# Performance work log

Measured on AMD Instinct MI355X. Metric: run time of the kernel, lower is better.

## Reference

```python
import jax, jax.numpy as jnp
import numpy as np

B, C, D, E = 2048, 64, 1024, 128
P_INT = 0.0  # p_int=0 -> intervention mask is all zeros (deterministic)


def setup_inputs() -> dict:
    key = jax.random.key(0)
    ks = jax.random.split(key, 16)
    s = lambda k, shape, fan: jax.random.normal(k, shape, jnp.float32) * (1.0 / np.sqrt(fan))
    return {
        "x": jax.random.normal(ks[0], (B, D), jnp.float32),
        "c_int": jax.random.uniform(ks[1], (B, C), jnp.float32),
        # stacked per-concept scorer MLP: Linear(D,D) -> ReLU -> Linear(D,1) -> Sigmoid
        "W1": s(ks[2], (C, D, D), D), "b1": jnp.zeros((C, D), jnp.float32),
        "w2": s(ks[3], (C, D), D), "b2": jnp.zeros((C,), jnp.float32),
        # stacked per-concept embed layer: Linear(D+1, D+1) -> ReLU
        "Wl": s(ks[4], (C, D + 1, D + 1), D + 1), "bl": jnp.zeros((C, D + 1), jnp.float32),
        # shared heads
        "Wmu": s(ks[5], (D + 1, E), D + 1), "bmu": jnp.zeros((E,), jnp.float32),
        "Wlv": s(ks[6], (D + 1, E), D + 1), "blv": jnp.zeros((E,), jnp.float32),
        "proto_pos": jax.random.normal(ks[7], (C, E), jnp.float32),
        "proto_neg": jax.random.normal(ks[8], (C, E), jnp.float32),
    }


def reference(x, c_int, W1, b1, w2, b2, Wl, bl, Wmu, bmu, Wlv, blv, proto_pos, proto_neg):
    # Concept scorers (all concepts batched as one grouped GEMM).
    h = jax.nn.relu(jnp.einsum("bd,cdk->bck", x, W1) + b1)          # [B,C,D]
    c_pred = jax.nn.sigmoid(jnp.einsum("bck,ck->bc", h, w2) + b2)    # [B,C]
    # Per-concept embedding layer on [x ; c_pred].
    xc = jnp.concatenate(
        [jnp.broadcast_to(x[:, None, :], (x.shape[0], C, D)), c_pred[..., None]], axis=-1
    )                                                                # [B,C,D+1]
    emb = jax.nn.relu(jnp.einsum("bck,ckj->bcj", xc, Wl) + bl)       # [B,C,D+1]
    mu = jnp.einsum("bcj,je->bce", emb, Wmu) + bmu                   # [B,C,E]
    logvar = jnp.einsum("bcj,je->bce", emb, Wlv) + blv               # [B,C,E]
    c_emb = mu  # eval mode: no reparameterization noise
    # Intervention blend (mask ~ Bernoulli(p_int); p_int=0 -> zeros, deterministic)
    mask = jnp.zeros_like(c_pred)                                    # [B,C]
    cp = mask * c_int + (1.0 - mask) * c_pred                        # [B,C]
    proto = cp[..., None] * proto_pos + (1.0 - cp[..., None]) * proto_neg  # [B,C,E]
    c_emb = mask[..., None] * proto + (1.0 - mask[..., None]) * c_emb
    return (c_pred, c_emb, mu, logvar)
```

## Files before the change

kernel.cpp:

```cpp
#include <hip/hip_runtime.h>
#include <hip/hip_bf16.h>
#include <cstdint>
#include <cstddef>

#define OFF_CE 131072ull
#define OFF_MU (131072ull + 16777216ull)
#define OFF_LV (131072ull + 33554432ull)

using bf16x8 = __attribute__((ext_vector_type(8))) __bf16;
using s16x8  = __attribute__((ext_vector_type(8))) short;
using f32x4  = __attribute__((ext_vector_type(4))) float;

__device__ __forceinline__ unsigned short f2bf(float x) {
  unsigned u = __builtin_bit_cast(unsigned, x);
  return (unsigned short)((u + 0x7FFFu + ((u >> 16) & 1u)) >> 16);
}
__device__ __forceinline__ float bf2f(unsigned short h) {
  unsigned u = ((unsigned)h) << 16;
  return __builtin_bit_cast(float, u);
}
__device__ __forceinline__ void async16(const void* g, void* l) {
  __builtin_amdgcn_global_load_lds(
      (const __attribute__((address_space(1))) void*)g,
      (__attribute__((address_space(3))) void*)l, 16, 0, 0);
}
__device__ __forceinline__ f32x4 nt_load4(const float* p4) {
  return __builtin_nontemporal_load((const f32x4*)p4);
}

struct PX {
  const float *b2, *presum, *w2l, *bl1024;
  float *e1024, *pred;
};

template <int ALIGNED>
__device__ __forceinline__ void tile_tr64_pair(
    const float* __restrict__ srcA, const float* __restrict__ srcB, int stride,
    unsigned short* __restrict__ dstA, unsigned short* __restrict__ dstB,
    int t256, float (*tA)[68], float (*tB)[68]) {
  const int row = t256 >> 4;
  const int col4 = (t256 & 15) << 2;
  f32x4 vA[4], vB[4];
#pragma unroll
  for (int i = 0; i < 4; ++i) {
    const float* q = srcA + (size_t)(row + (i << 4)) * stride + col4;
    if constexpr (ALIGNED) {
      vA[i] = nt_load4(q);
    } else {
      vA[i].x = __builtin_nontemporal_load(q);
      vA[i].y = __builtin_nontemporal_load(q + 1);
      vA[i].z = __builtin_nontemporal_load(q + 2);
      vA[i].w = __builtin_nontemporal_load(q + 3);
    }
  }
#pragma unroll
  for (int i = 0; i < 4; ++i) {
    const float* q = srcB + (size_t)(row + (i << 4)) * stride + col4;
    if constexpr (ALIGNED) {
      vB[i] = nt_load4(q);
    } else {
      vB[i].x = __builtin_nontemporal_load(q);
      vB[i].y = __builtin_nontemporal_load(q + 1);
      vB[i].z = __builtin_nontemporal_load(q + 2);
      vB[i].w = __builtin_nontemporal_load(q + 3);
    }
  }
#pragma unroll
  for (int i = 0; i < 4; ++i) *(f32x4*)&tA[row + (i << 4)][col4] = vA[i];
  __syncthreads();
#pragma unroll
  for (int i = 0; i < 4; ++i) *(f32x4*)&tB[row + (i << 4)][col4] = vB[i];
  const int n = t256 & 63;
#pragma unroll
  for (int pq = 0; pq < 2; ++pq) {
    const int k8 = ((t256 >> 6) << 3) + (pq << 5);
    unsigned short tmp[8];
#pragma unroll
    for (int j = 0; j < 8; ++j) tmp[j] = f2bf(tA[k8 + j][n]);
    *(uint4*)(dstA + (size_t)n * 1024 + k8) = *(uint4*)tmp;
  }
  __syncthreads();
#pragma unroll
  for (int pq = 0; pq < 2; ++pq) {
    const int k8 = ((t256 >> 6) << 3) + (pq << 5);
    unsigned short tmp[8];
#pragma unroll
    for (int j = 0; j < 8; ++j) tmp[j] = f2bf(tB[k8 + j][n]);
    *(uint4*)(dstB + (size_t)n * 1024 + k8) = *(uint4*)tmp;
  }
}

__global__ __launch_bounds__(512) void prep1_k(const float* __restrict__ W1,
                                               const float* __restrict__ x,
                                               const float* __restrict__ Wl,
                                               const float* __restrict__ bl,
                                               unsigned short* __restrict__ xb,
                                               unsigned short* __restrict__ W1T,
                                               float* __restrict__ wlastf,
                                               float* __restrict__ blpf,
                                               float* __restrict__ Wlcolf,
                                               float* __restrict__ w2l,
                                               float* __restrict__ bl1024) {
  __shared__ float t[4][64][68];
  const int bid = blockIdx.x;
  const int tid = threadIdx.x;
  if (bid < 4096) {
    const int g = tid >> 8, t256 = tid & 255;
    const int tau0 = (bid << 2) + (g << 1);
    const int c0 = tau0 >> 8, kt0 = (tau0 >> 4) & 15, nt0 = tau0 & 15;
    const int tau1 = tau0 + 1;
    const int c1 = tau1 >> 8, kt1 = (tau1 >> 4) & 15, nt1 = tau1 & 15;
    tile_tr64_pair<1>(
        W1 + ((size_t)c0 << 20) + ((size_t)(kt0 << 6) << 10) + (nt0 << 6),
        W1 + ((size_t)c1 << 20) + ((size_t)(kt1 << 6) << 10) + (nt1 << 6), 1024,
        W1T + ((size_t)c0 << 20) + ((size_t)(nt0 << 6) << 10) + (kt0 << 6),
        W1T + ((size_t)c1 << 20) + ((size_t)(nt1 << 6) << 10) + (kt1 << 6),
        t256, t[g << 1], t[(g << 1) + 1]);
  } else if (bid < 4608) {
    const int idx = (bid - 4096) * 512 + tid;
    f32x4 a = nt_load4(x + (size_t)idx * 8);
    f32x4 b = nt_load4(x + (size_t)idx * 8 + 4);
    unsigned w0 = f2bf(a.x) | ((unsigned)f2bf(a.y) << 16);
    unsigned w1 = f2bf(a.z) | ((unsigned)f2bf(a.w) << 16);
    unsigned w2 = f2bf(b.x) | ((unsigned)f2bf(b.y) << 16);
    unsigned w3 = f2bf(b.z) | ((unsigned)f2bf(b.w) << 16);
    ((uint4*)xb)[idx] = make_uint4(w0, w1, w2, w3);
  } else {
    const int idx = (bid - 4608) * 512 + tid;
    const int c = idx >> 10, j = idx & 1023;
    const float* src = Wl + (size_t)c * 1050625;
    wlastf[idx] = __builtin_nontemporal_load(&src[(size_t)1024 * 1025 + j]);
    blpf[idx]   = bl[(size_t)c * 1025 + j];
    Wlcolf[idx] = __builtin_nontemporal_load(&src[(size_t)j * 1025 + 1024]);
    if (j == 0) {
      w2l[c]    = src[(size_t)1024 * 1025 + 1024];
      bl1024[c] = bl[(size_t)c * 1025 + 1024];
    }
  }
}

__global__ __launch_bounds__(512) void wl2_k(const float* __restrict__ Wl,
                                             const float* __restrict__ Wmu,
                                             const float* __restrict__ Wlv,
                                             const unsigned short* __restrict__ xb,
                                             const float* __restrict__ Wlcolf,
                                             unsigned short* __restrict__ WlT,
                                             unsigned short* __restrict__ WheadT,
                                             float* __restrict__ whead1024f,
                                             float* __restrict__ presum) {
  __shared__ float t[4][64][68];
  const int bid = blockIdx.x;
  const int tid = threadIdx.x;
  if (bid < 4096) {
    const int g = tid >> 8, t256 = tid & 255;
    const int tau0 = (bid << 2) + (g << 1);
    const int c0 = tau0 >> 8, kt0 = (tau0 >> 4) & 15, nt0 = tau0 & 15;
    const int tau1 = tau0 + 1;
    const int c1 = tau1 >> 8, kt1 = (tau1 >> 4) & 15, nt1 = tau1 & 15;
    tile_tr64_pair<0>(
        Wl + (size_t)c0 * 1050625 + (size_t)(kt0 << 6) * 1025 + (nt0 << 6),
        Wl + (size_t)c1 * 1050625 + (size_t)(kt1 << 6) * 1025 + (nt1 << 6), 1025,
        WlT + ((size_t)c0 << 20) + ((size_t)(nt0 << 6) << 10) + (kt0 << 6),
        WlT + ((size_t)c1 << 20) + ((size_t)(nt1 << 6) << 10) + (kt1 << 6),
        t256, t[g << 1], t[(g << 1) + 1]);
  } else if (bid < 4608) {
    const int we = bid - 4096;
    const int idx = we * 512 + tid;
    const int rr = idx >> 10, k = idx & 1023;
    float v = (rr < 128) ? Wmu[(size_t)k * 128 + rr] : Wlv[(size_t)k * 128 + (rr - 128)];
    WheadT[idx] = f2bf(v);
    if (we == 0 && tid < 256)
      whead1024f[tid] = (tid < 128) ? Wmu[131072 + tid] : Wlv[131072 + (tid - 128)];
  } else {
    const int b = bid - 4608;
    const int w = tid >> 6, lane = tid & 63;
    const unsigned short* xr = xb + ((size_t)b << 10) + lane * 16;
    s16x8 xv0 = *(const s16x8*)xr;
    s16x8 xv1 = *(const s16x8*)(xr + 8);
    float xf[16];
#pragma unroll
    for (int i = 0; i < 8; ++i) {
      xf[i] = bf2f((unsigned short)xv0[i]);
      xf[8 + i] = bf2f((unsigned short)xv1[i]);
    }
#pragma unroll
    for (int q = 0; q < 8; ++q) {
      const int c = (q << 3) + w;
      const float* wr = Wlcolf + (c << 10) + lane * 16;
      float s = 0.f;
#pragma unroll
      for (int q4 = 0; q4 < 4; ++q4) {
        f32x4 wv = *(const f32x4*)(wr + q4 * 4);
        s += xf[q4 * 4 + 0] * wv.x + xf[q4 * 4 + 1] * wv.y +
             xf[q4 * 4 + 2] * wv.z + xf[q4 * 4 + 3] * wv.w;
      }
#pragma unroll
      for (int off = 32; off; off >>= 1) s += __shfl_xor(s, off);
      if (lane == 0) presum[(c << 11) + b] = s;
    }
  }
}


#define BAR() __builtin_amdgcn_s_barrier()
#define LGKM0() do { asm volatile("s_waitcnt lgkmcnt(0)" ::: "memory"); \
                     __builtin_amdgcn_sched_barrier(0); } while (0)
#define VM4() asm volatile("s_waitcnt vmcnt(4)" ::: "memory")
#define VM0() asm volatile("s_waitcnt vmcnt(0)" ::: "memory")

#define STAGEA(h, tt, bidx) do { _Pragma("unroll") for (int q_ = 0; q_ < 2; ++q_) \
  async16(Asrc[q_] + ((size_t)(h) * 128) * K + (size_t)(tt) * 64, \
          &sA[bidx][(h) * 8192 + chnk[q_]]); } while (0)
#define STAGEB(h, tt, bidx) do { _Pragma("unroll") for (int q_ = 0; q_ < 2; ++q_) \
  async16(Bsrc[q_] + ((size_t)(h) * 128) * K + (size_t)(tt) * 64, \
          &sB[bidx][(h) * 8192 + chnk[q_]]); } while (0)

#define LOADA(mh, bidx) do { _Pragma("unroll") for (int i_ = 0; i_ < 4; ++i_) { \
  const int ro_ = ((mh) * 128 + wm64 + i_ * 16 + l15) << 6; \
  a[i_][0] = *(const bf16x8*)&sA[bidx][ro_ + ccx0]; \
  a[i_][1] = *(const bf16x8*)&sA[bidx][ro_ + ccx1]; } } while (0)

#define LOADB(nh, bb, bidx) do { _Pragma("unroll") for (int j_ = 0; j_ < 2; ++j_) { \
  const int ro_ = ((nh) * 128 + wn32 + j_ * 16 + l15) << 6; \
  bb[j_][0] = *(const bf16x8*)&sB[bidx][ro_ + ccx0]; \
  bb[j_][1] = *(const bf16x8*)&sB[bidx][ro_ + ccx1]; } } while (0)

#define MMAQ(mh, nh, bb) do { _Pragma("unroll") for (int i_ = 0; i_ < 4; ++i_) \
  _Pragma("unroll") for (int j_ = 0; j_ < 2; ++j_) { \
    acc[(mh)*4+i_][(nh)*2+j_] = __builtin_amdgcn_mfma_f32_16x16x32_bf16( \
        a[i_][0], bb[j_][0], acc[(mh)*4+i_][(nh)*2+j_], 0, 0, 0); \
    acc[(mh)*4+i_][(nh)*2+j_] = __builtin_amdgcn_mfma_f32_16x16x32_bf16( \
        a[i_][1], bb[j_][1], acc[(mh)*4+i_][(nh)*2+j_], 0, 0, 0); \
  } } while (0)

#define KSTEP(t_, cb_, nb_) do { \
    LOADA(0, cb_); LOADB(0, b0, cb_); STAGEA(0, (t_) + 1, nb_); \
    BAR(); LGKM0(); \
    __builtin_amdgcn_s_setprio(1); MMAQ(0, 0, b0); __builtin_amdgcn_s_setprio(0); \
    VM4(); BAR(); \
    LOADB(1, b1, cb_); STAGEB(0, (t_) + 1, nb_); \
    BAR(); LGKM0(); \
    __builtin_amdgcn_s_setprio(1); MMAQ(0, 1, b1); __builtin_amdgcn_s_setprio(0); \
    VM4(); BAR(); \
    LOADA(1, cb_); STAGEB(1, (t_) + 1, nb_); \
    BAR(); LGKM0(); \
    __builtin_amdgcn_s_setprio(1); MMAQ(1, 1, b1); __builtin_amdgcn_s_setprio(0); \
    BAR(); \
    STAGEA(1, (t_) + 1, nb_); \
    BAR(); \
    __builtin_amdgcn_s_setprio(1); MMAQ(1, 0, b0); __builtin_amdgcn_s_setprio(0); \
    VM4(); BAR(); \
  } while (0)

template <int MODE, int K>
__global__ __launch_bounds__(512, 2) void gemm8p_k(
    const unsigned short* __restrict__ A, const unsigned short* __restrict__ BT,
    const float* __restrict__ e0, const float* __restrict__ e1,
    const float* __restrict__ e2, const float* __restrict__ e3,
    unsigned short* __restrict__ obf, float* __restrict__ ofl, PX p) {
  __shared__ unsigned short sA[2][16384];
  __shared__ unsigned short sB[2][16384];

  constexpr int GX = (MODE == 2) ? 1 : 4;
  constexpr int GY = (MODE == 2) ? 512 : 8;
  constexpr int NWG = GX * GY * ((MODE == 2) ? 1 : 64);

  const int tid = threadIdx.x;
  const int lane = tid & 63;
  const int wid = tid >> 6;
  const int wm = wid >> 2, wn = wid & 3;
  const int l15 = lane & 15, l4 = lane >> 4;
  const int wm64 = wm << 6, wn32 = wn << 5;

  const int rbid = blockIdx.x + GX * (blockIdx.y + GY * blockIdx.z);
  const int bid = (rbid & 7) * (NWG >> 3) + (rbid >> 3);
  const int bx = bid % GX;
  const int by = (bid / GX) % GY;
  const int c = bid / (GX * GY);

  const int n0 = bx << 8;
  const int m0 = by << 8;

  const unsigned short* Ab = A;
  const unsigned short* Bb;
  if constexpr (MODE == 2) Bb = BT;
  else                     Bb = BT + ((size_t)c << 20);

  int rloc[2], csrc[2], chnk[2];
  const unsigned short* Asrc[2];
  const unsigned short* Bsrc[2];
#pragma unroll
  for (int q = 0; q < 2; ++q) {
    const int s = ((wid << 1) + q) * 64 + lane;
    rloc[q] = s >> 3;
    csrc[q] = ((s & 7) ^ ((s >> 3) & 7)) << 3;
    chnk[q] = ((wid << 1) + q) << 9;
    Asrc[q] = Ab + (size_t)(m0 + rloc[q]) * K + csrc[q];
    Bsrc[q] = Bb + (size_t)(n0 + rloc[q]) * K + csrc[q];
  }

  const int xorv = l15 & 7;
  const int ccx0 = (l4 ^ xorv) << 3;
  const int ccx1 = ((4 + l4) ^ xorv) << 3;

  f32x4 acc[8][4];
#pragma unroll
  for (int i = 0; i < 8; ++i)
#pragma unroll
    for (int j = 0; j < 4; ++j) acc[i][j] = (f32x4)(0.f);

  bf16x8 a[4][2], b0[2][2], b1[2][2];

  static_assert(K == 1024, "schedule assumes 16 K-tiles");

  STAGEA(0, 0, 0); STAGEB(0, 0, 0); STAGEB(1, 0, 0); STAGEA(1, 0, 0);
  VM0();
  BAR();

#pragma unroll 1
  for (int tt = 0; tt < 7; ++tt) {
    const int t0 = tt << 1;
    KSTEP(t0, 0, 1);
    KSTEP(t0 + 1, 1, 0);
  }
  KSTEP(14, 0, 1);

  {
    VM0();
    BAR();
    LOADA(0, 1);
    LOADB(0, b0, 1);
    LGKM0();
    __builtin_amdgcn_s_setprio(1);
    MMAQ(0, 0, b0);
    __builtin_amdgcn_s_setprio(0);
    LOADB(1, b1, 1);
    LGKM0();
    __builtin_amdgcn_s_setprio(1);
    MMAQ(0, 1, b1);
    __builtin_amdgcn_s_setprio(0);
    LOADA(1, 1);
    LGKM0();
    __builtin_amdgcn_s_setprio(1);
    MMAQ(1, 1, b1);
    MMAQ(1, 0, b0);
    __builtin_amdgcn_s_setprio(0);
  }

  int coln[2][2];
#pragma unroll
  for (int nh = 0; nh < 2; ++nh)
#pragma unroll
    for (int j = 0; j < 2; ++j) coln[nh][j] = n0 + nh * 128 + wn32 + j * 16 + l15;

  if constexpr (MODE == 0) {
    float bias[2][2], w2v[2][2];
#pragma unroll
    for (int nh = 0; nh < 2; ++nh)
#pragma unroll
      for (int j = 0; j < 2; ++j) {
        bias[nh][j] = e0[(c << 10) + coln[nh][j]];
        w2v[nh][j]  = e1[(c << 10) + coln[nh][j]];
      }
    float* partL = (float*)&sA[0][0];
#pragma unroll
    for (int mh = 0; mh < 2; ++mh)
#pragma unroll
      for (int i = 0; i < 4; ++i)
#pragma unroll
        for (int rr = 0; rr < 4; ++rr) {
          float s = 0.f;
#pragma unroll
          for (int nh = 0; nh < 2; ++nh)
#pragma unroll
            for (int j = 0; j < 2; ++j) {
              float v = fmaxf(acc[mh * 4 + i][nh * 2 + j][rr] + bias[nh][j], 0.f);
              s += v * w2v[nh][j];
            }
          s += __shfl_xor(s, 1); s += __shfl_xor(s, 2);
          s += __shfl_xor(s, 4); s += __shfl_xor(s, 8);
          if (l15 == 0) partL[wid * 128 + mh * 64 + i * 16 + (l4 << 2) + rr] = s;
        }
    __syncthreads();
    if (tid < 256) {
      const int r = tid;
      const int mh_ = r >> 7, wmr = (r >> 6) & 1, low = r & 63;
      float s2 = 0.f;
#pragma unroll
      for (int wn2 = 0; wn2 < 4; ++wn2) s2 += partL[(wmr * 4 + wn2) * 128 + mh_ * 64 + low];
      ofl[(((size_t)(bx << 6) + c) << 11) + m0 + r] = s2;
    }
  } else if constexpr (MODE == 1) {
    float* cpL = (float*)&sA[0][0];
    if (tid < 256) {
      const int b = m0 + tid;
      float s = p.b2[c];
#pragma unroll
      for (int q = 0; q < 4; ++q) s += e2[(((size_t)(q << 6) + c) << 11) + b];
      float pv = 1.f / (1.f + expf(-s));
      cpL[tid] = pv;
      if (bx == 0) {
        p.pred[((size_t)b << 6) + c] = pv;
        p.e1024[(c << 11) + b] =
            fmaxf(p.presum[(c << 11) + b] + pv * p.w2l[c] + p.bl1024[c], 0.f);
      }
    }
    __syncthreads();
    float wl4[2][2], bb4[2][2];
#pragma unroll
    for (int nh = 0; nh < 2; ++nh)
#pragma unroll
      for (int j = 0; j < 2; ++j) {
        wl4[nh][j] = e0[(c << 10) + coln[nh][j]];
        bb4[nh][j] = e1[(c << 10) + coln[nh][j]];
      }
#pragma unroll
    for (int mh = 0; mh < 2; ++mh)
#pragma unroll
      for (int i = 0; i < 4; ++i)
#pragma unroll
        for (int rr = 0; rr < 4; ++rr) {
          const int rl = mh * 128 + wm64 + i * 16 + (l4 << 2) + rr;
          const int row = m0 + rl;
          const float cp = cpL[rl];
          unsigned short* orow = obf + (((size_t)(c << 11) + row) << 10);
#pragma unroll
          for (int nh = 0; nh < 2; ++nh)
#pragma unroll
            for (int j = 0; j < 2; ++j) {
              float v = acc[mh * 4 + i][nh * 2 + j][rr] + cp * wl4[nh][j] + bb4[nh][j];
              orow[coln[nh][j]] = f2bf(fmaxf(v, 0.f));
            }
        }
  } else {
    float bias[2][2], wh[2][2];
#pragma unroll
    for (int nh = 0; nh < 2; ++nh)
#pragma unroll
      for (int j = 0; j < 2; ++j) {
        bias[nh][j] = (nh == 0) ? e0[coln[0][j]] : e1[coln[1][j] - 128];
        wh[nh][j]   = e3[coln[nh][j]];
      }
#pragma unroll
    for (int mh = 0; mh < 2; ++mh)
#pragma unroll
      for (int i = 0; i < 4; ++i)
#pragma unroll
        for (int rr = 0; rr < 4; ++rr) {
          const int rid = m0 + mh * 128 + wm64 + i * 16 + (l4 << 2) + rr;
          const int cc = rid >> 11, b = rid & 2047;
          const float ev = e2[rid];
          const size_t ib = (((size_t)b << 6) + cc) << 7;
#pragma unroll
          for (int j = 0; j < 2; ++j) {
            float v = acc[mh * 4 + i][j][rr] + bias[0][j] + ev * wh[0][j];
            ofl[OFF_MU + ib + coln[0][j]] = v;
            ofl[OFF_CE + ib + coln[0][j]] = v;
          }
#pragma unroll
          for (int j = 0; j < 2; ++j) {
            float v = acc[mh * 4 + i][2 + j][rr] + bias[1][j] + ev * wh[1][j];
            ofl[OFF_LV + ib + (coln[1][j] - 128)] = v;
          }
        }
  }
}


extern "C" void kernel_launch(void* const* d_in, const int* in_sizes, int n_in,
                              void* d_out, int out_size, void* d_ws, size_t ws_size,
                              hipStream_t stream) {
  const float* x   = (const float*)d_in[0];
  const float* W1  = (const float*)d_in[2];
  const float* b1  = (const float*)d_in[3];
  const float* w2  = (const float*)d_in[4];
  const float* b2  = (const float*)d_in[5];
  const float* Wl  = (const float*)d_in[6];
  const float* bl  = (const float*)d_in[7];
  const float* Wmu = (const float*)d_in[8];
  const float* bmu = (const float*)d_in[9];
  const float* Wlv = (const float*)d_in[10];
  const float* blv = (const float*)d_in[11];
  float* out = (float*)d_out;

  char* ws = (char*)d_ws;
  size_t off = 0;
  auto take = [&](size_t bytes) { char* r = ws + off; off += bytes; return r; };
  unsigned short* xb     = (unsigned short*)take(4194304);
  unsigned short* W1T    = (unsigned short*)take(134217728);
  unsigned short* WlT    = (unsigned short*)take(134217728);
  float* wlastf          = (float*)take(262144);
  float* blpf            = (float*)take(262144);
  float* Wlcolf          = (float*)take(262144);
  float* w2l             = (float*)take(512);
  float* bl1024          = (float*)take(512);
  unsigned short* WheadT = (unsigned short*)take(524288);
  float* whead1024f      = (float*)take(1024);
  float* presum          = (float*)take(524288);
  float* spart           = (float*)take(2097152);
  float* e1024f          = (float*)take(524288);
  unsigned short* emb    = (unsigned short*)take(268435456);

  PX p;
  p.b2 = b2; p.presum = presum; p.w2l = w2l; p.bl1024 = bl1024;
  p.e1024 = e1024f; p.pred = out;

  prep1_k<<<4736, 512, 0, stream>>>(W1, x, Wl, bl, xb, W1T, wlastf, blpf, Wlcolf, w2l, bl1024);
  gemm8p_k<0, 1024><<<dim3(4, 8, 64), 512, 0, stream>>>(xb, W1T, b1, w2, nullptr, nullptr,
                                                        nullptr, spart, p);
  wl2_k<<<6656, 512, 0, stream>>>(Wl, Wmu, Wlv, xb, Wlcolf, WlT, WheadT, whead1024f, presum);
  gemm8p_k<1, 1024><<<dim3(4, 8, 64), 512, 0, stream>>>(xb, WlT, wlastf, blpf, spart, nullptr,
                                                        emb, nullptr, p);
  gemm8p_k<2, 1024><<<dim3(1, 512, 1), 512, 0, stream>>>(emb, WheadT, bmu, blv, e1024f,
                                                         whead1024f, nullptr, out, p);
}
```

Baseline: 948.8 us.

## Fold Wl transpose and head prep into the first GEMM launch as tail blocks

The separate wl2_k launch (Wl transpose to bf16, head weight transpose, presum dot products) is merged into the MODE 0 GEMM launch as extra blocks beyond index 2048, reusing the GEMM's shared memory as scratch. This removes one kernel launch boundary and lets the memory-bound transpose work run on CUs that become free while GEMM blocks finish, overlapping the two stages. The tail blocks are scheduled after the GEMM blocks, so overlap depends on dispatch order. The mixed block types also share one kernel's register and LDS budget, which could affect occupancy.

```diff
diff --git a/kernel.cpp b/kernel.cpp
--- a/kernel.cpp
+++ b/kernel.cpp
@@ -29,8 +29,10 @@
 }
 
 struct PX {
-  const float *b2, *presum, *w2l, *bl1024;
-  float *e1024, *pred;
+  const float *Wl, *Wmu, *Wlv, *b2, *w2l, *bl1024, *Wlcolf;
+  const unsigned short *xb;
+  unsigned short *WlT, *WheadT;
+  float *whead1024f, *presum, *e1024, *pred;
 };
 
 template <int ALIGNED>
@@ -139,65 +141,56 @@
   }
 }
 
-__global__ __launch_bounds__(512) void wl2_k(const float* __restrict__ Wl,
-                                             const float* __restrict__ Wmu,
-                                             const float* __restrict__ Wlv,
-                                             const unsigned short* __restrict__ xb,
-                                             const float* __restrict__ Wlcolf,
-                                             unsigned short* __restrict__ WlT,
-                                             unsigned short* __restrict__ WheadT,
-                                             float* __restrict__ whead1024f,
-                                             float* __restrict__ presum) {
-  __shared__ float t[4][64][68];
-  const int bid = blockIdx.x;
-  const int tid = threadIdx.x;
-  if (bid < 4096) {
+__device__ void tail_work(int e, int tid, char* lds, const PX& p) {
+  if (e < 4096) {
     const int g = tid >> 8, t256 = tid & 255;
-    const int tau0 = (bid << 2) + (g << 1);
+    const int tau0 = (e << 2) + (g << 1);
     const int c0 = tau0 >> 8, kt0 = (tau0 >> 4) & 15, nt0 = tau0 & 15;
     const int tau1 = tau0 + 1;
     const int c1 = tau1 >> 8, kt1 = (tau1 >> 4) & 15, nt1 = tau1 & 15;
     tile_tr64_pair<0>(
-        Wl + (size_t)c0 * 1050625 + (size_t)(kt0 << 6) * 1025 + (nt0 << 6),
-        Wl + (size_t)c1 * 1050625 + (size_t)(kt1 << 6) * 1025 + (nt1 << 6), 1025,
-        WlT + ((size_t)c0 << 20) + ((size_t)(nt0 << 6) << 10) + (kt0 << 6),
-        WlT + ((size_t)c1 << 20) + ((size_t)(nt1 << 6) << 10) + (kt1 << 6),
-        t256, t[g << 1], t[(g << 1) + 1]);
-  } else if (bid < 4608) {
-    const int we = bid - 4096;
+        p.Wl + (size_t)c0 * 1050625 + (size_t)(kt0 << 6) * 1025 + (nt0 << 6),
+        p.Wl + (size_t)c1 * 1050625 + (size_t)(kt1 << 6) * 1025 + (nt1 << 6), 1025,
+        p.WlT + ((size_t)c0 << 20) + ((size_t)(nt0 << 6) << 10) + (kt0 << 6),
+        p.WlT + ((size_t)c1 << 20) + ((size_t)(nt1 << 6) << 10) + (kt1 << 6),
+        t256, (float(*)[68])(lds + g * 34816), (float(*)[68])(lds + g * 34816 + 17408));
+    return;
+  }
+  if (e < 4608) {
+    const int we = e - 4096;
     const int idx = we * 512 + tid;
     const int rr = idx >> 10, k = idx & 1023;
-    float v = (rr < 128) ? Wmu[(size_t)k * 128 + rr] : Wlv[(size_t)k * 128 + (rr - 128)];
-    WheadT[idx] = f2bf(v);
+    float v = (rr < 128) ? p.Wmu[(size_t)k * 128 + rr] : p.Wlv[(size_t)k * 128 + (rr - 128)];
+    p.WheadT[idx] = f2bf(v);
     if (we == 0 && tid < 256)
-      whead1024f[tid] = (tid < 128) ? Wmu[131072 + tid] : Wlv[131072 + (tid - 128)];
-  } else {
-    const int b = bid - 4608;
-    const int w = tid >> 6, lane = tid & 63;
-    const unsigned short* xr = xb + ((size_t)b << 10) + lane * 16;
-    s16x8 xv0 = *(const s16x8*)xr;
-    s16x8 xv1 = *(const s16x8*)(xr + 8);
-    float xf[16];
-#pragma unroll
-    for (int i = 0; i < 8; ++i) {
-      xf[i] = bf2f((unsigned short)xv0[i]);
-      xf[8 + i] = bf2f((unsigned short)xv1[i]);
+      p.whead1024f[tid] = (tid < 128) ? p.Wmu[131072 + tid] : p.Wlv[131072 + (tid - 128)];
+    return;
+  }
+  const int b = e - 4608;
+  const int w = tid >> 6, lane = tid & 63;
+  const unsigned short* xr = p.xb + ((size_t)b << 10) + lane * 16;
+  s16x8 xv0 = *(const s16x8*)xr;
+  s16x8 xv1 = *(const s16x8*)(xr + 8);
+  float xf[16];
+#pragma unroll
+  for (int i = 0; i < 8; ++i) {
+    xf[i] = bf2f((unsigned short)xv0[i]);
+    xf[8 + i] = bf2f((unsigned short)xv1[i]);
+  }
+#pragma unroll
+  for (int q = 0; q < 8; ++q) {
+    const int c = (q << 3) + w;
+    const float* wr = p.Wlcolf + (c << 10) + lane * 16;
+    float s = 0.f;
+#pragma unroll
+    for (int q4 = 0; q4 < 4; ++q4) {
+      f32x4 wv = *(const f32x4*)(wr + q4 * 4);
+      s += xf[q4 * 4 + 0] * wv.x + xf[q4 * 4 + 1] * wv.y +
+           xf[q4 * 4 + 2] * wv.z + xf[q4 * 4 + 3] * wv.w;
     }
 #pragma unroll
-    for (int q = 0; q < 8; ++q) {
-      const int c = (q << 3) + w;
-      const float* wr = Wlcolf + (c << 10) + lane * 16;
-      float s = 0.f;
-#pragma unroll
-      for (int q4 = 0; q4 < 4; ++q4) {
-        f32x4 wv = *(const f32x4*)(wr + q4 * 4);
-        s += xf[q4 * 4 + 0] * wv.x + xf[q4 * 4 + 1] * wv.y +
-             xf[q4 * 4 + 2] * wv.z + xf[q4 * 4 + 3] * wv.w;
-      }
-#pragma unroll
-      for (int off = 32; off; off >>= 1) s += __shfl_xor(s, off);
-      if (lane == 0) presum[(c << 11) + b] = s;
-    }
+    for (int off = 32; off; off >>= 1) s += __shfl_xor(s, off);
+    if (lane == 0) p.presum[(c << 11) + b] = s;
   }
 }
 
@@ -266,13 +259,22 @@
   constexpr int NWG = GX * GY * ((MODE == 2) ? 1 : 64);
 
   const int tid = threadIdx.x;
+
+  int rbid;
+  if constexpr (MODE == 0) {
+    const int bidR = blockIdx.x;
+    if (bidR >= 2048) { tail_work(bidR - 2048, tid, (char*)&sA[0][0], p); return; }
+    rbid = bidR;
+  } else {
+    rbid = blockIdx.x + GX * (blockIdx.y + GY * blockIdx.z);
+  }
+
   const int lane = tid & 63;
   const int wid = tid >> 6;
   const int wm = wid >> 2, wn = wid & 3;
   const int l15 = lane & 15, l4 = lane >> 4;
   const int wm64 = wm << 6, wn32 = wn << 5;
 
-  const int rbid = blockIdx.x + GX * (blockIdx.y + GY * blockIdx.z);
   const int bid = (rbid & 7) * (NWG >> 3) + (rbid >> 3);
   const int bx = bid % GX;
   const int by = (bid / GX) % GY;
@@ -502,13 +504,14 @@
   unsigned short* emb    = (unsigned short*)take(268435456);
 
   PX p;
-  p.b2 = b2; p.presum = presum; p.w2l = w2l; p.bl1024 = bl1024;
-  p.e1024 = e1024f; p.pred = out;
+  p.Wl = Wl; p.Wmu = Wmu; p.Wlv = Wlv; p.b2 = b2;
+  p.w2l = w2l; p.bl1024 = bl1024; p.Wlcolf = Wlcolf;
+  p.xb = xb; p.WlT = WlT; p.WheadT = WheadT;
+  p.whead1024f = whead1024f; p.presum = presum; p.e1024 = e1024f; p.pred = out;
 
   prep1_k<<<4736, 512, 0, stream>>>(W1, x, Wl, bl, xb, W1T, wlastf, blpf, Wlcolf, w2l, bl1024);
-  gemm8p_k<0, 1024><<<dim3(4, 8, 64), 512, 0, stream>>>(xb, W1T, b1, w2, nullptr, nullptr,
-                                                        nullptr, spart, p);
-  wl2_k<<<6656, 512, 0, stream>>>(Wl, Wmu, Wlv, xb, Wlcolf, WlT, WheadT, whead1024f, presum);
+  gemm8p_k<0, 1024><<<8704, 512, 0, stream>>>(xb, W1T, b1, w2, nullptr, nullptr,
+                                              nullptr, spart, p);
   gemm8p_k<1, 1024><<<dim3(4, 8, 64), 512, 0, stream>>>(xb, WlT, wlastf, blpf, spart, nullptr,
                                                         emb, nullptr, p);
   gemm8p_k<2, 1024><<<dim3(1, 512, 1), 512, 0, stream>>>(emb, WheadT, bmu, blv, e1024f,
```

After: 961.9 us. Within noise of the previous version (+1.4%).
